# Optimization experiments

Measured on AMD Instinct MI355X. Metric: run time of the kernel, lower is better.

The kernel has to match this reference:

```python
import jax, jax.numpy as jnp
import numpy as np

IN_SIZE = 4096   # input_size
OUT_SIZE = 4096  # output_size
RANK = 1024      # len(S_4), multiple of 32
GROUPSIZE = 128
BITS = 4
PACK = 32 // BITS  # 8 nibbles per int32
MAXQ_MASK = (1 << BITS) - 1  # 15


def _dequant4(qweight, qzeros, scales, g_idx):
    """GPTQ 4-bit dequant. qweight: int32 [K//8, N]; qzeros: int32 [G, N//8];
    scales: [G, N]; g_idx: int32 [K]. Returns W [K, N] with
    W[k, n] = (int4[k, n] - (zero4[g_idx[k], n] + 1)) * scales[g_idx[k], n]."""
    shifts = (jnp.arange(PACK, dtype=jnp.int32) * BITS)
    K = qweight.shape[0] * PACK
    N = qweight.shape[1]
    # unpack along rows: [K//8, 8, N] -> [K, N]
    intw = ((qweight[:, None, :] >> shifts[None, :, None]) & MAXQ_MASK).reshape(K, N)
    # unpack along cols: [G, N//8, 8] -> [G, N]; pack() stored zeros-1, so add 1 back
    zeros = ((qzeros[:, :, None] >> shifts[None, None, :]) & MAXQ_MASK).reshape(qzeros.shape[0], N) + 1
    sc = scales[g_idx]            # [K, N]
    zr = zeros[g_idx].astype(scales.dtype)  # [K, N]
    return (intw.astype(scales.dtype) - zr) * sc


def setup_inputs() -> dict:
    key = jax.random.key(0)
    ks = jax.random.split(key, 9)
    qweight_V = jax.random.randint(ks[0], (IN_SIZE // PACK, RANK), 0, 2**31 - 1, dtype=jnp.int32)
    qzeros_V = jax.random.randint(ks[1], (IN_SIZE // GROUPSIZE, RANK // PACK), 0, 2**31 - 1, dtype=jnp.int32)
    scales_V = jax.random.uniform(ks[2], (IN_SIZE // GROUPSIZE, RANK), dtype=jnp.float32) * 0.01 + 1e-3
    g_idx_V = (jnp.arange(IN_SIZE, dtype=jnp.int32) // GROUPSIZE).astype(jnp.int32)
    qweight_U = jax.random.randint(ks[3], (RANK // PACK, OUT_SIZE), 0, 2**31 - 1, dtype=jnp.int32)
    qzeros_U = jax.random.randint(ks[4], (RANK // GROUPSIZE, OUT_SIZE // PACK), 0, 2**31 - 1, dtype=jnp.int32)
    scales_U = jax.random.uniform(ks[5], (RANK // GROUPSIZE, OUT_SIZE), dtype=jnp.float32) * 0.01 + 1e-3
    g_idx_U = (jnp.arange(RANK, dtype=jnp.int32) // GROUPSIZE).astype(jnp.int32)
    S = jax.random.uniform(ks[6], (RANK,), dtype=jnp.float32) + 0.1  # singular values
    x = jax.random.normal(ks[7], (4, 2048, IN_SIZE), dtype=jnp.float32)
    return {"x": x,
            "qweight_V": qweight_V, "qzeros_V": qzeros_V, "scales_V": scales_V, "g_idx_V": g_idx_V,
            "qweight_U": qweight_U, "qzeros_U": qzeros_U, "scales_U": scales_U, "g_idx_U": g_idx_U,
            "S": S}


def reference(x, qweight_V, qzeros_V, scales_V, g_idx_V,
              qweight_U, qzeros_U, scales_U, g_idx_U, S):
    # weight_V: dequantized [IN_SIZE, RANK]; weight_U: dequantized [RANK, OUT_SIZE]
    weight_V = _dequant4(qweight_V, qzeros_V, scales_V, g_idx_V)
    weight_U = _dequant4(qweight_U, qzeros_U, scales_U, g_idx_U)
    # forward returns (weight_V @ diag(S) @ weight_U).T  -> [OUT_SIZE, IN_SIZE]
    # (the x @ W_V @ diag(S) @ W_U activation path in the source is dead code
    #  w.r.t. the returned value)
    return ((weight_V * S[None, :]) @ weight_U).T
```

## Files before the change

kernel.cpp:

```cpp
#include <hip/hip_runtime.h>

typedef __attribute__((ext_vector_type(8))) short bf16x8;
typedef __attribute__((ext_vector_type(4))) float f32x4;

__device__ __forceinline__ short f2bf(float f) {
  unsigned u = __builtin_bit_cast(unsigned, f);
  u += 0x7fffu + ((u >> 16) & 1u);
  return (short)(u >> 16);
}


__global__ __launch_bounds__(256) void dequant_v(const int* __restrict__ qw,
                                                 const int* __restrict__ qz,
                                                 const float* __restrict__ sc,
                                                 const float* __restrict__ S,
                                                 short* __restrict__ P) {
  const int t  = blockIdx.x * 256 + threadIdx.x;
  const int r8 = t & 127;
  const int k  = t >> 7;
  const int g  = k >> 7;
  const int kw = k >> 3;
  const int sh = (k & 7) << 2;
  const int r0 = r8 << 3;
  const int zw = qz[(g << 7) + r8];
  const int*   wq  = qw + kw * 1024 + r0;
  const float* scp = sc + (g << 10) + r0;
  const float* sp  = S + r0;
  bf16x8 res;
#pragma unroll
  for (int i = 0; i < 8; ++i) {
    int q = (wq[i] >> sh) & 15;
    int z = ((zw >> (i << 2)) & 15) + 1;
    res[i] = f2bf((float)(q - z) * scp[i] * sp[i]);
  }
  *(bf16x8*)(P + (k << 10) + r0) = res;
}

__global__ __launch_bounds__(256) void dequant_u(const int* __restrict__ qw,
                                                 const int* __restrict__ qz,
                                                 const float* __restrict__ sc,
                                                 short* __restrict__ Qt) {
  const int t  = blockIdx.x * 256 + threadIdx.x;
  const int rw = t & 127;
  const int n  = t >> 7;
  const int g  = rw >> 4;
  const int w  = qw[(rw << 12) + n];
  const int zw = qz[(g << 9) + (n >> 3)];
  const int z  = ((zw >> ((n & 7) << 2)) & 15) + 1;
  const float s = sc[(g << 12) + n];
  bf16x8 res;
#pragma unroll
  for (int i = 0; i < 8; ++i) {
    int q = (w >> (i << 2)) & 15;
    res[i] = f2bf((float)(q - z) * s);
  }
  *(bf16x8*)(Qt + (n << 10) + (rw << 3)) = res;
}

#define GLL(g, l)                                                              \
  __builtin_amdgcn_global_load_lds(                                            \
      (const __attribute__((address_space(1))) void*)(g),                      \
      (__attribute__((address_space(3))) void*)(l), 16, 0, 0)

__global__ __launch_bounds__(512, 2) void gemm256(const short* __restrict__ P,
                                                  const short* __restrict__ Qt,
                                                  float* __restrict__ out) {
  __shared__ __align__(16) char lds[131072];
  const int tid  = threadIdx.x;
  const int lane = tid & 63;
  const int wid  = tid >> 6;
  const int wm   = wid >> 2;
  const int wn   = wid & 3;
  const int m0 = (blockIdx.x >> 4) << 8;
  const int n0 = (blockIdx.x & 15) << 8;

  const int srow = tid >> 3;
  const int scol = ((tid & 7) << 4) ^ ((srow & 7) << 4);
  const short* pA[4];
  const short* pB[4];
#pragma unroll
  for (int r = 0; r < 4; ++r) {
    pA[r] = P  + (m0 + r * 64 + srow) * 1024 + (scol >> 1);
    pB[r] = Qt + (n0 + r * 64 + srow) * 1024 + (scol >> 1);
  }

#define STAGE(b, kt) do {                                                      \
    const int kb_ = (kt) << 6;                                                 \
    _Pragma("unroll")                                                          \
    for (int r_ = 0; r_ < 4; ++r_)                                             \
      GLL(pA[r_] + kb_, lds + (b) * 65536 + r_ * 8192 + wid * 1024);           \
    _Pragma("unroll")                                                          \
    for (int r_ = 0; r_ < 4; ++r_)                                             \
      GLL(pB[r_] + kb_, lds + (b) * 65536 + 32768 + r_ * 8192 + wid * 1024);   \
  } while (0)

  const int ra   = ((wm << 7) + (lane & 15)) << 7;
  const int rb   = ((wn << 6) + (lane & 15)) << 7;
  const int swz  = (lane & 7) << 4;
  const int offk0 = (((lane >> 4) << 4)) ^ swz;
  const int offk1 = (64 + ((lane >> 4) << 4)) ^ swz;

  f32x4 acc[8][4];
#pragma unroll
  for (int mi = 0; mi < 8; ++mi)
#pragma unroll
    for (int ni = 0; ni < 4; ++ni) acc[mi][ni] = f32x4{0.f, 0.f, 0.f, 0.f};

  STAGE(0, 0);
  STAGE(1, 1);

  int cur = 0;
  for (int kt = 0; kt < 16; ++kt) {
    if (kt == 15) asm volatile("s_waitcnt vmcnt(0)" ::: "memory");
    else          asm volatile("s_waitcnt vmcnt(8)" ::: "memory");
    __builtin_amdgcn_s_barrier();
    __builtin_amdgcn_sched_barrier(0);

    const char* Ab = lds + cur * 65536;
    const char* Bb = Ab + 32768;
#pragma unroll
    for (int kk = 0; kk < 2; ++kk) {
      const int offk = kk ? offk1 : offk0;
      bf16x8 bfr[4], afr[8];
#pragma unroll
      for (int ni = 0; ni < 4; ++ni)
        bfr[ni] = *(const bf16x8*)(Bb + rb + ni * 2048 + offk);
#pragma unroll
      for (int mi = 0; mi < 8; ++mi)
        afr[mi] = *(const bf16x8*)(Ab + ra + mi * 2048 + offk);
      __builtin_amdgcn_s_setprio(1);
#pragma unroll
      for (int mi = 0; mi < 8; ++mi)
#pragma unroll
        for (int ni = 0; ni < 4; ++ni)
          acc[mi][ni] = __builtin_amdgcn_mfma_f32_16x16x32_bf16(
              afr[mi], bfr[ni], acc[mi][ni], 0, 0, 0);
      __builtin_amdgcn_s_setprio(0);
    }

    asm volatile("s_waitcnt lgkmcnt(0)" ::: "memory");
    __builtin_amdgcn_s_barrier();
    if (kt < 14) STAGE(cur, kt + 2);
    cur ^= 1;
  }

  const int mbase = m0 + (wm << 7) + ((lane >> 4) << 2);
  const int nbase = n0 + (wn << 6) + (lane & 15);
#pragma unroll
  for (int mi = 0; mi < 8; ++mi)
#pragma unroll
    for (int ni = 0; ni < 4; ++ni)
      *(f32x4*)(out + (size_t)(nbase + ni * 16) * 4096 + mbase + mi * 16) =
          acc[mi][ni];
#undef STAGE
}

extern "C" void kernel_launch(void* const* d_in, const int* in_sizes, int n_in,
                              void* d_out, int out_size, void* d_ws, size_t ws_size,
                              hipStream_t stream) {
  const int*   qw_V = (const int*)d_in[1];
  const int*   qz_V = (const int*)d_in[2];
  const float* sc_V = (const float*)d_in[3];
  const int*   qw_U = (const int*)d_in[5];
  const int*   qz_U = (const int*)d_in[6];
  const float* sc_U = (const float*)d_in[7];
  const float* S    = (const float*)d_in[9];

  short* P  = (short*)d_ws;
  short* Qt = (short*)d_ws + 4096 * 1024;
  float* out = (float*)d_out;

  dequant_v<<<2048, 256, 0, stream>>>(qw_V, qz_V, sc_V, S, P);
  dequant_u<<<2048, 256, 0, stream>>>(qw_U, qz_U, sc_U, Qt);
  gemm256<<<256, 512, 0, stream>>>(P, Qt, out);
}
```

Before: 57.93 us.

## Split GEMM k-step into four quadrant phases interleaving LDS reads and prefetch

Restructures the GEMM main loop so each k-tile runs as four MFMA quadrant phases (A-top/B-left, A-top/B-right, A-bottom/B-right, A-bottom/B-left). LDS fragment reads happen per phase, and each half of the next tile's global-to-LDS prefetch is issued as soon as that buffer half is no longer needed. The goal is to overlap LDS traffic and global loads with MFMA work and to lower fragment register pressure. The cost is extra barriers per iteration and a more fragile wait-count and barrier schedule.

```diff
diff --git a/kernel.cpp b/kernel.cpp
--- a/kernel.cpp
+++ b/kernel.cpp
@@ -76,29 +76,22 @@
 
   const int srow = tid >> 3;
   const int scol = ((tid & 7) << 4) ^ ((srow & 7) << 4);
-  const short* pA[4];
-  const short* pB[4];
-#pragma unroll
-  for (int r = 0; r < 4; ++r) {
-    pA[r] = P  + (m0 + r * 64 + srow) * 1024 + (scol >> 1);
-    pB[r] = Qt + (n0 + r * 64 + srow) * 1024 + (scol >> 1);
-  }
-
-#define STAGE(b, kt) do {                                                      \
-    const int kb_ = (kt) << 6;                                                 \
-    _Pragma("unroll")                                                          \
-    for (int r_ = 0; r_ < 4; ++r_)                                             \
-      GLL(pA[r_] + kb_, lds + (b) * 65536 + r_ * 8192 + wid * 1024);           \
-    _Pragma("unroll")                                                          \
-    for (int r_ = 0; r_ < 4; ++r_)                                             \
-      GLL(pB[r_] + kb_, lds + (b) * 65536 + 32768 + r_ * 8192 + wid * 1024);   \
+  const short* gA = P  + (m0 + srow) * 1024 + (scol >> 1);
+  const short* gB = Qt + (n0 + srow) * 1024 + (scol >> 1);
+
+#define STG(gp, roff, half, ktv) do {                                          \
+    const short* s_ = (gp) + (half) * 131072 + ((ktv) << 6);                   \
+    char* d_ = lds + (roff) + (half) * 16384 + (wid << 10);                    \
+    GLL(s_, d_);                                                               \
+    GLL(s_ + 65536, d_ + 8192);                                                \
   } while (0)
 
-  const int ra   = ((wm << 7) + (lane & 15)) << 7;
-  const int rb   = ((wn << 6) + (lane & 15)) << 7;
+  const int arow_b = ((wm << 7) + (lane & 15)) << 7;
+  const int brow_b = ((wn << 6) + (lane & 15)) << 7;
+  const int klo  = (lane >> 4) << 4;
   const int swz  = (lane & 7) << 4;
-  const int offk0 = (((lane >> 4) << 4)) ^ swz;
-  const int offk1 = (64 + ((lane >> 4) << 4)) ^ swz;
+  const int offk0 = klo ^ swz;
+  const int offk1 = (klo | 64) ^ swz;
 
   f32x4 acc[8][4];
 #pragma unroll
@@ -106,42 +99,107 @@
 #pragma unroll
     for (int ni = 0; ni < 4; ++ni) acc[mi][ni] = f32x4{0.f, 0.f, 0.f, 0.f};
 
-  STAGE(0, 0);
-  STAGE(1, 1);
-
-  int cur = 0;
+  bf16x8 ah[4][2], bh0[2][2], bh1[2][2];
+
+  STG(gA, 0, 0, 0);
+  STG(gA, 0, 1, 0);
+  STG(gB, 32768, 0, 0);
+  STG(gB, 32768, 1, 0);
+  STG(gA, 65536, 0, 1);
+  STG(gA, 65536, 1, 1);
+  STG(gB, 65536 + 32768, 0, 1);
+  STG(gB, 65536 + 32768, 1, 1);
+  asm volatile("s_waitcnt vmcnt(8)" ::: "memory");
+  __builtin_amdgcn_s_barrier();
+
   for (int kt = 0; kt < 16; ++kt) {
-    if (kt == 15) asm volatile("s_waitcnt vmcnt(0)" ::: "memory");
+    const int curbuf = (kt & 1) << 16;
+    const char* Ab = lds + curbuf;
+    const char* Bb = Ab + 32768;
+
+#pragma unroll
+    for (int i = 0; i < 4; ++i) {
+      ah[i][0] = *(const bf16x8*)(Ab + arow_b + i * 2048 + offk0);
+      ah[i][1] = *(const bf16x8*)(Ab + arow_b + i * 2048 + offk1);
+    }
+#pragma unroll
+    for (int j = 0; j < 2; ++j) {
+      bh0[j][0] = *(const bf16x8*)(Bb + brow_b + j * 2048 + offk0);
+      bh0[j][1] = *(const bf16x8*)(Bb + brow_b + j * 2048 + offk1);
+    }
+    asm volatile("s_waitcnt lgkmcnt(0)" ::: "memory");
+    __builtin_amdgcn_sched_barrier(0);
+    __builtin_amdgcn_s_setprio(1);
+#pragma unroll
+    for (int kk = 0; kk < 2; ++kk)
+#pragma unroll
+      for (int i = 0; i < 4; ++i)
+#pragma unroll
+        for (int j = 0; j < 2; ++j)
+          acc[i][j] = __builtin_amdgcn_mfma_f32_16x16x32_bf16(
+              ah[i][kk], bh0[j][kk], acc[i][j], 0, 0, 0);
+    __builtin_amdgcn_s_setprio(0);
+    __builtin_amdgcn_s_barrier();
+
+#pragma unroll
+    for (int j = 0; j < 2; ++j) {
+      bh1[j][0] = *(const bf16x8*)(Bb + brow_b + 4096 + j * 2048 + offk0);
+      bh1[j][1] = *(const bf16x8*)(Bb + brow_b + 4096 + j * 2048 + offk1);
+    }
+    asm volatile("s_waitcnt lgkmcnt(0)" ::: "memory");
+    __builtin_amdgcn_sched_barrier(0);
+    __builtin_amdgcn_s_setprio(1);
+#pragma unroll
+    for (int kk = 0; kk < 2; ++kk)
+#pragma unroll
+      for (int i = 0; i < 4; ++i)
+#pragma unroll
+        for (int j = 0; j < 2; ++j)
+          acc[i][2 + j] = __builtin_amdgcn_mfma_f32_16x16x32_bf16(
+              ah[i][kk], bh1[j][kk], acc[i][2 + j], 0, 0, 0);
+    __builtin_amdgcn_s_setprio(0);
+    __builtin_amdgcn_s_barrier();
+
+#pragma unroll
+    for (int i = 0; i < 4; ++i) {
+      ah[i][0] = *(const bf16x8*)(Ab + arow_b + 8192 + i * 2048 + offk0);
+      ah[i][1] = *(const bf16x8*)(Ab + arow_b + 8192 + i * 2048 + offk1);
+    }
+    if (kt < 14) {
+      STG(gB, curbuf + 32768, 0, kt + 2);
+      STG(gB, curbuf + 32768, 1, kt + 2);
+    }
+    asm volatile("s_waitcnt lgkmcnt(0)" ::: "memory");
+    __builtin_amdgcn_sched_barrier(0);
+    __builtin_amdgcn_s_setprio(1);
+#pragma unroll
+    for (int kk = 0; kk < 2; ++kk)
+#pragma unroll
+      for (int i = 0; i < 4; ++i)
+#pragma unroll
+        for (int j = 0; j < 2; ++j)
+          acc[4 + i][2 + j] = __builtin_amdgcn_mfma_f32_16x16x32_bf16(
+              ah[i][kk], bh1[j][kk], acc[4 + i][2 + j], 0, 0, 0);
+    __builtin_amdgcn_s_setprio(0);
+    __builtin_amdgcn_s_barrier();
+
+    if (kt < 14) {
+      STG(gA, curbuf, 0, kt + 2);
+      STG(gA, curbuf, 1, kt + 2);
+    }
+    __builtin_amdgcn_s_setprio(1);
+#pragma unroll
+    for (int kk = 0; kk < 2; ++kk)
+#pragma unroll
+      for (int i = 0; i < 4; ++i)
+#pragma unroll
+        for (int j = 0; j < 2; ++j)
+          acc[4 + i][j] = __builtin_amdgcn_mfma_f32_16x16x32_bf16(
+              ah[i][kk], bh0[j][kk], acc[4 + i][j], 0, 0, 0);
+    __builtin_amdgcn_s_setprio(0);
+    if (kt == 14) asm volatile("s_waitcnt vmcnt(0)" ::: "memory");
     else          asm volatile("s_waitcnt vmcnt(8)" ::: "memory");
     __builtin_amdgcn_s_barrier();
-    __builtin_amdgcn_sched_barrier(0);
-
-    const char* Ab = lds + cur * 65536;
-    const char* Bb = Ab + 32768;
-#pragma unroll
-    for (int kk = 0; kk < 2; ++kk) {
-      const int offk = kk ? offk1 : offk0;
-      bf16x8 bfr[4], afr[8];
-#pragma unroll
-      for (int ni = 0; ni < 4; ++ni)
-        bfr[ni] = *(const bf16x8*)(Bb + rb + ni * 2048 + offk);
-#pragma unroll
-      for (int mi = 0; mi < 8; ++mi)
-        afr[mi] = *(const bf16x8*)(Ab + ra + mi * 2048 + offk);
-      __builtin_amdgcn_s_setprio(1);
-#pragma unroll
-      for (int mi = 0; mi < 8; ++mi)
-#pragma unroll
-        for (int ni = 0; ni < 4; ++ni)
-          acc[mi][ni] = __builtin_amdgcn_mfma_f32_16x16x32_bf16(
-              afr[mi], bfr[ni], acc[mi][ni], 0, 0, 0);
-      __builtin_amdgcn_s_setprio(0);
-    }
-
-    asm volatile("s_waitcnt lgkmcnt(0)" ::: "memory");
-    __builtin_amdgcn_s_barrier();
-    if (kt < 14) STAGE(cur, kt + 2);
-    cur ^= 1;
   }
 
   const int mbase = m0 + (wm << 7) + ((lane >> 4) << 2);
@@ -152,7 +210,7 @@
     for (int ni = 0; ni < 4; ++ni)
       *(f32x4*)(out + (size_t)(nbase + ni * 16) * 4096 + mbase + mi * 16) =
           acc[mi][ni];
-#undef STAGE
+#undef STG
 }
 
 extern "C" void kernel_launch(void* const* d_in, const int* in_sizes, int n_in,
```

After: 55.05 us. -5.0%, faster.
